# Optimization experiments

Hardware: AMD Instinct MI355X
Metric: run time of the kernel (lower is better)

Reference implementation:

```python
import jax, jax.numpy as jnp
import numpy as np

N = 8192
IN_F = 512
OUT_F = 256
EDGE_P = 0.02  # adjacency density


def setup_inputs() -> dict:
    key = jax.random.key(0)
    k1, k2, k3, k4 = jax.random.split(key, 4)
    x = jax.random.normal(k1, (N, IN_F), dtype=jnp.float32)
    # xavier_uniform with gain=1.414 ~ std gain*sqrt(2/(fan_in+fan_out))
    W = jax.random.normal(k2, (IN_F, OUT_F), dtype=jnp.float32) * (1.414 * np.sqrt(2.0 / (IN_F + OUT_F)))
    a = jax.random.normal(k3, (2 * OUT_F, 1), dtype=jnp.float32) * (1.414 * np.sqrt(2.0 / (2 * OUT_F + 1)))
    adj = (jax.random.uniform(k4, (N, N)) < EDGE_P).astype(jnp.float32)
    return {"x": x, "adj": adj, "W": W, "a": a}


def reference(x, adj, W, a):
    h = x @ W                        # [N, F]
    F = h.shape[1]
    # repeat/cat reduces to an outer sum of two [N] vectors.
    s_src = (h @ a[:F]).squeeze(-1)  # [N], contribution of h_i
    s_dst = (h @ a[F:]).squeeze(-1)  # [N], contribution of h_j
    e = jax.nn.leaky_relu(s_src[:, None] + s_dst[None, :], negative_slope=0.2)  # [N, N]
    # NOTE: original code softmaxes over the FULL row, THEN multiplies by adj.
    attention = jax.nn.softmax(e, axis=1) * adj  # [N, N]
    h_prime = attention @ h                      # [N, F]
    return h_prime, attention
```

## Files before the change

### kernel.cpp

```cpp
#include <hip/hip_runtime.h>
#include <hip/hip_bf16.h>

#define N_NODES 8192
#define IN_F    512
#define OUT_F   256
#define MAXNZ   512

typedef float v4f  __attribute__((ext_vector_type(4)));
typedef __attribute__((ext_vector_type(8)))  short bf16x8;
typedef __attribute__((ext_vector_type(16))) float f32x16;
typedef unsigned short u16;
typedef unsigned int   u32;

__device__ __forceinline__ u16 f2bf(float f) {
  u32 u = __float_as_uint(f);
  u += 0x7fffu + ((u >> 16) & 1u);
  return (u16)(u >> 16);
}
__device__ __forceinline__ float bf2f(u16 h) {
  return __uint_as_float(((u32)h) << 16);
}

__global__ __launch_bounds__(256) void k_cast_x(const float* __restrict__ x,
                                                u16* __restrict__ x_hi,
                                                u16* __restrict__ x_lo) {
  const int idx = blockIdx.x * 256 + threadIdx.x;
  const float4 v = ((const float4*)x)[idx];
  u16 h0 = f2bf(v.x), h1 = f2bf(v.y), h2 = f2bf(v.z), h3 = f2bf(v.w);
  u16 l0 = f2bf(v.x - bf2f(h0)), l1 = f2bf(v.y - bf2f(h1));
  u16 l2 = f2bf(v.z - bf2f(h2)), l3 = f2bf(v.w - bf2f(h3));
  uint2 hp, lp;
  hp.x = (u32)h0 | ((u32)h1 << 16); hp.y = (u32)h2 | ((u32)h3 << 16);
  lp.x = (u32)l0 | ((u32)l1 << 16); lp.y = (u32)l2 | ((u32)l3 << 16);
  ((uint2*)x_hi)[idx] = hp;
  ((uint2*)x_lo)[idx] = lp;
}

__global__ __launch_bounds__(256) void k_cast_wt(const float* __restrict__ W,
                                                 u16* __restrict__ wt_hi,
                                                 u16* __restrict__ wt_lo) {
  const int k = blockIdx.x;
  const int n = threadIdx.x;
  const float v = W[(size_t)k * OUT_F + n];
  const u16 h = f2bf(v);
  wt_hi[(size_t)n * IN_F + k] = h;
  wt_lo[(size_t)n * IN_F + k] = f2bf(v - bf2f(h));
}

#define GBK 64
__global__ __launch_bounds__(256) void k_gemm_mfma(const u16* __restrict__ x_hi,
                                                   const u16* __restrict__ x_lo,
                                                   const u16* __restrict__ wt_hi,
                                                   const u16* __restrict__ wt_lo,
                                                   const float* __restrict__ a,
                                                   u16* __restrict__ h_bf,
                                                   float* __restrict__ s_src,
                                                   float* __restrict__ s_dst) {
  __shared__ u16 As_hi[64 * 68], As_lo[64 * 68], Bs_hi[64 * 68], Bs_lo[64 * 68];
  const int t    = threadIdx.x;
  const int bn   = blockIdx.x & 3;
  const int bm   = blockIdx.x >> 2;
  const int m0   = bm * 64, n0 = bn * 64;
  const int lane = t & 63;
  const int w    = t >> 6;
  const int wm   = w & 1, wn = w >> 1;

  const int sm = t >> 2;
  const int sk = (t & 3) * 16;

  f32x16 acc = {};

  for (int k0 = 0; k0 < IN_F; k0 += GBK) {
#pragma unroll
    for (int i = 0; i < 2; ++i) {
      const int ko = sk + i * 8;
      *(bf16x8*)&As_hi[sm * 68 + ko] = *(const bf16x8*)&x_hi[(size_t)(m0 + sm) * IN_F + k0 + ko];
      *(bf16x8*)&As_lo[sm * 68 + ko] = *(const bf16x8*)&x_lo[(size_t)(m0 + sm) * IN_F + k0 + ko];
      *(bf16x8*)&Bs_hi[sm * 68 + ko] = *(const bf16x8*)&wt_hi[(size_t)(n0 + sm) * IN_F + k0 + ko];
      *(bf16x8*)&Bs_lo[sm * 68 + ko] = *(const bf16x8*)&wt_lo[(size_t)(n0 + sm) * IN_F + k0 + ko];
    }
    __syncthreads();
    const int am  = wm * 32 + (lane & 31);
    const int bn_ = wn * 32 + (lane & 31);
#pragma unroll
    for (int kk = 0; kk < 4; ++kk) {
      const int ko = kk * 16 + (lane >> 5) * 8;
      const bf16x8 ah = *(const bf16x8*)&As_hi[am * 68 + ko];
      const bf16x8 al = *(const bf16x8*)&As_lo[am * 68 + ko];
      const bf16x8 bh = *(const bf16x8*)&Bs_hi[bn_ * 68 + ko];
      const bf16x8 bl = *(const bf16x8*)&Bs_lo[bn_ * 68 + ko];
      acc = __builtin_amdgcn_mfma_f32_32x32x16_bf16(ah, bh, acc, 0, 0, 0);
      acc = __builtin_amdgcn_mfma_f32_32x32x16_bf16(al, bh, acc, 0, 0, 0);
      acc = __builtin_amdgcn_mfma_f32_32x32x16_bf16(ah, bl, acc, 0, 0, 0);
    }
    __syncthreads();
  }
  const int colg = n0 + wn * 32 + (lane & 31);
  const float asv = a[colg];
  const float adv = a[OUT_F + colg];
#pragma unroll
  for (int r = 0; r < 16; ++r) {
    const int row = m0 + wm * 32 + (r & 3) + 8 * (r >> 2) + 4 * (lane >> 5);
    const float v = acc[r];
    h_bf[(size_t)row * OUT_F + colg] = f2bf(v);
    float vs = v * asv, vd = v * adv;
#pragma unroll
    for (int off = 1; off < 32; off <<= 1) {
      vs += __shfl_xor(vs, off);
      vd += __shfl_xor(vd, off);
    }
    if ((lane & 31) == 0) {
      atomicAdd(&s_src[row], vs);
      atomicAdd(&s_dst[row], vd);
    }
  }
}

__device__ __forceinline__ float lrelu_exp(float v) {
  const float e = v > 0.f ? v : 0.2f * v;
  return __expf(e);
}

__global__ __launch_bounds__(256) void k_attn(const float* __restrict__ adj,
                                              const u16* __restrict__ h_bf,
                                              const float* __restrict__ s_src,
                                              const float* __restrict__ s_dst,
                                              float* __restrict__ out_hp,
                                              float* __restrict__ out_att) {
  __shared__ float nza[MAXNZ];
  __shared__ int   nzj[MAXNZ];
  __shared__ float redbuf[4];
  __shared__ int   cnt;

  const int t = threadIdx.x;
  const int i = blockIdx.x;
  const float ssrc = s_src[i];
  if (t == 0) cnt = 0;

  const float4* sd4 = (const float4*)s_dst;
  float4 p[8];
  float lsum = 0.f;
#pragma unroll
  for (int c = 0; c < 8; ++c) {
    const float4 s = sd4[c * 256 + t];
    p[c].x = lrelu_exp(ssrc + s.x);
    p[c].y = lrelu_exp(ssrc + s.y);
    p[c].z = lrelu_exp(ssrc + s.z);
    p[c].w = lrelu_exp(ssrc + s.w);
    lsum += p[c].x + p[c].y + p[c].z + p[c].w;
  }
#pragma unroll
  for (int off = 32; off > 0; off >>= 1) lsum += __shfl_down(lsum, off);
  if ((t & 63) == 0) redbuf[t >> 6] = lsum;
  __syncthreads();
  const float inv = 1.0f / (redbuf[0] + redbuf[1] + redbuf[2] + redbuf[3]);

  const v4f* adj4 = (const v4f*)(adj + (size_t)i * N_NODES);
  v4f*       att4 = (v4f*)(out_att + (size_t)i * N_NODES);
  v4f av[8];
#pragma unroll
  for (int c = 0; c < 8; ++c) av[c] = __builtin_nontemporal_load(adj4 + c * 256 + t);
#pragma unroll
  for (int c = 0; c < 8; ++c) {
    v4f att;
    att.x = av[c].x * (p[c].x * inv);
    att.y = av[c].y * (p[c].y * inv);
    att.z = av[c].z * (p[c].z * inv);
    att.w = av[c].w * (p[c].w * inv);
    __builtin_nontemporal_store(att, att4 + c * 256 + t);
    const int j = (c * 256 + t) * 4;
    if (av[c].x != 0.f) { const int k = atomicAdd(&cnt, 1); if (k < MAXNZ) { nzj[k] = j + 0; nza[k] = att.x; } }
    if (av[c].y != 0.f) { const int k = atomicAdd(&cnt, 1); if (k < MAXNZ) { nzj[k] = j + 1; nza[k] = att.y; } }
    if (av[c].z != 0.f) { const int k = atomicAdd(&cnt, 1); if (k < MAXNZ) { nzj[k] = j + 2; nza[k] = att.z; } }
    if (av[c].w != 0.f) { const int k = atomicAdd(&cnt, 1); if (k < MAXNZ) { nzj[k] = j + 3; nza[k] = att.w; } }
  }
  __syncthreads();

  const int n = cnt < MAXNZ ? cnt : MAXNZ;
  float acc = 0.f;
#pragma unroll 8
  for (int k = 0; k < n; ++k) {
    acc = fmaf(nza[k], bf2f(h_bf[(size_t)nzj[k] * OUT_F + t]), acc);
  }
  out_hp[(size_t)i * OUT_F + t] = acc;
}

extern "C" void kernel_launch(void* const* d_in, const int* in_sizes, int n_in,
                              void* d_out, int out_size, void* d_ws, size_t ws_size,
                              hipStream_t stream) {
  const float* x   = (const float*)d_in[0];
  const float* adj = (const float*)d_in[1];
  const float* W   = (const float*)d_in[2];
  const float* a   = (const float*)d_in[3];

  float* out_hp  = (float*)d_out;
  float* out_att = (float*)d_out + (size_t)N_NODES * OUT_F;

  char* ws = (char*)d_ws;
  float* ssrc_ws = (float*)ws;                       ws += N_NODES * 4;
  float* sdst_ws = (float*)ws;                       ws += N_NODES * 4;
  u16*   x_hi    = (u16*)ws;                         ws += (size_t)N_NODES * IN_F * 2;
  u16*   x_lo    = (u16*)ws;                         ws += (size_t)N_NODES * IN_F * 2;
  u16*   wt_hi   = (u16*)ws;                         ws += (size_t)OUT_F * IN_F * 2;
  u16*   wt_lo   = (u16*)ws;                         ws += (size_t)OUT_F * IN_F * 2;
  u16*   h_bf    = (u16*)ws;                         ws += (size_t)N_NODES * OUT_F * 2;

  hipMemsetAsync(ssrc_ws, 0, 2 * N_NODES * sizeof(float), stream);

  k_cast_x<<<(N_NODES * IN_F / 4) / 256, 256, 0, stream>>>(x, x_hi, x_lo);
  k_cast_wt<<<IN_F, OUT_F, 0, stream>>>(W, wt_hi, wt_lo);
  k_gemm_mfma<<<(N_NODES / 64) * (OUT_F / 64), 256, 0, stream>>>(
      x_hi, x_lo, wt_hi, wt_lo, a, h_bf, ssrc_ws, sdst_ws);
  k_attn<<<N_NODES, 256, 0, stream>>>(adj, h_bf, ssrc_ws, sdst_ws, out_hp, out_att);
}
```

Baseline: 508.1 us.

## Assign one wavefront per attention row and recompute exp instead of caching

The attention kernel now maps each 64-lane wavefront to its own row, so a 256-thread block handles four rows. This removes block-wide __syncthreads and the shared-memory reduction; the softmax sum is reduced with wave shuffles only. Exponentials are computed in a first pass for the sum and computed again in a second pass, which cuts register use but doubles the exp work and the s_dst reads. The sparse aggregation now has each lane accumulate four output features from 8-byte h loads and write them as one float4.

```diff
diff --git a/kernel.cpp b/kernel.cpp
--- a/kernel.cpp
+++ b/kernel.cpp
@@ -127,62 +127,72 @@
                                               const float* __restrict__ s_dst,
                                               float* __restrict__ out_hp,
                                               float* __restrict__ out_att) {
-  __shared__ float nza[MAXNZ];
-  __shared__ int   nzj[MAXNZ];
-  __shared__ float redbuf[4];
-  __shared__ int   cnt;
-
-  const int t = threadIdx.x;
-  const int i = blockIdx.x;
+  __shared__ float nza[4][MAXNZ];
+  __shared__ int   nzj[4][MAXNZ];
+  __shared__ int   cnt[4];
+
+  const int lane = threadIdx.x & 63;
+  const int wid  = threadIdx.x >> 6;
+  const int i    = blockIdx.x * 4 + wid;
   const float ssrc = s_src[i];
-  if (t == 0) cnt = 0;
+  if (lane == 0) cnt[wid] = 0;
 
   const float4* sd4 = (const float4*)s_dst;
-  float4 p[8];
+
   float lsum = 0.f;
-#pragma unroll
-  for (int c = 0; c < 8; ++c) {
-    const float4 s = sd4[c * 256 + t];
-    p[c].x = lrelu_exp(ssrc + s.x);
-    p[c].y = lrelu_exp(ssrc + s.y);
-    p[c].z = lrelu_exp(ssrc + s.z);
-    p[c].w = lrelu_exp(ssrc + s.w);
-    lsum += p[c].x + p[c].y + p[c].z + p[c].w;
+  for (int c0 = 0; c0 < 32; c0 += 4) {
+    float4 s[4];
+#pragma unroll
+    for (int u = 0; u < 4; ++u) s[u] = sd4[(c0 + u) * 64 + lane];
+#pragma unroll
+    for (int u = 0; u < 4; ++u) {
+      lsum += lrelu_exp(ssrc + s[u].x) + lrelu_exp(ssrc + s[u].y)
+            + lrelu_exp(ssrc + s[u].z) + lrelu_exp(ssrc + s[u].w);
+    }
   }
 #pragma unroll
   for (int off = 32; off > 0; off >>= 1) lsum += __shfl_down(lsum, off);
-  if ((t & 63) == 0) redbuf[t >> 6] = lsum;
-  __syncthreads();
-  const float inv = 1.0f / (redbuf[0] + redbuf[1] + redbuf[2] + redbuf[3]);
+  const float inv = 1.0f / __shfl(lsum, 0);
 
   const v4f* adj4 = (const v4f*)(adj + (size_t)i * N_NODES);
   v4f*       att4 = (v4f*)(out_att + (size_t)i * N_NODES);
-  v4f av[8];
-#pragma unroll
-  for (int c = 0; c < 8; ++c) av[c] = __builtin_nontemporal_load(adj4 + c * 256 + t);
-#pragma unroll
-  for (int c = 0; c < 8; ++c) {
-    v4f att;
-    att.x = av[c].x * (p[c].x * inv);
-    att.y = av[c].y * (p[c].y * inv);
-    att.z = av[c].z * (p[c].z * inv);
-    att.w = av[c].w * (p[c].w * inv);
-    __builtin_nontemporal_store(att, att4 + c * 256 + t);
-    const int j = (c * 256 + t) * 4;
-    if (av[c].x != 0.f) { const int k = atomicAdd(&cnt, 1); if (k < MAXNZ) { nzj[k] = j + 0; nza[k] = att.x; } }
-    if (av[c].y != 0.f) { const int k = atomicAdd(&cnt, 1); if (k < MAXNZ) { nzj[k] = j + 1; nza[k] = att.y; } }
-    if (av[c].z != 0.f) { const int k = atomicAdd(&cnt, 1); if (k < MAXNZ) { nzj[k] = j + 2; nza[k] = att.z; } }
-    if (av[c].w != 0.f) { const int k = atomicAdd(&cnt, 1); if (k < MAXNZ) { nzj[k] = j + 3; nza[k] = att.w; } }
-  }
-  __syncthreads();
-
-  const int n = cnt < MAXNZ ? cnt : MAXNZ;
-  float acc = 0.f;
+  for (int c0 = 0; c0 < 32; c0 += 4) {
+    v4f   av[4];
+    float4 s[4];
+#pragma unroll
+    for (int u = 0; u < 4; ++u) av[u] = __builtin_nontemporal_load(adj4 + (c0 + u) * 64 + lane);
+#pragma unroll
+    for (int u = 0; u < 4; ++u) s[u] = sd4[(c0 + u) * 64 + lane];
+#pragma unroll
+    for (int u = 0; u < 4; ++u) {
+      v4f att;
+      att.x = av[u].x * (lrelu_exp(ssrc + s[u].x) * inv);
+      att.y = av[u].y * (lrelu_exp(ssrc + s[u].y) * inv);
+      att.z = av[u].z * (lrelu_exp(ssrc + s[u].z) * inv);
+      att.w = av[u].w * (lrelu_exp(ssrc + s[u].w) * inv);
+      __builtin_nontemporal_store(att, att4 + (c0 + u) * 64 + lane);
+      const int j = ((c0 + u) * 64 + lane) * 4;
+      if (av[u].x != 0.f) { const int k = atomicAdd(&cnt[wid], 1); if (k < MAXNZ) { nzj[wid][k] = j + 0; nza[wid][k] = att.x; } }
+      if (av[u].y != 0.f) { const int k = atomicAdd(&cnt[wid], 1); if (k < MAXNZ) { nzj[wid][k] = j + 1; nza[wid][k] = att.y; } }
+      if (av[u].z != 0.f) { const int k = atomicAdd(&cnt[wid], 1); if (k < MAXNZ) { nzj[wid][k] = j + 2; nza[wid][k] = att.z; } }
+      if (av[u].w != 0.f) { const int k = atomicAdd(&cnt[wid], 1); if (k < MAXNZ) { nzj[wid][k] = j + 3; nza[wid][k] = att.w; } }
+    }
+  }
+
+  const int n = cnt[wid] < MAXNZ ? cnt[wid] : MAXNZ;
+  float a0 = 0.f, a1 = 0.f, a2 = 0.f, a3 = 0.f;
 #pragma unroll 8
   for (int k = 0; k < n; ++k) {
-    acc = fmaf(nza[k], bf2f(h_bf[(size_t)nzj[k] * OUT_F + t]), acc);
-  }
-  out_hp[(size_t)i * OUT_F + t] = acc;
+    const int   j = nzj[wid][k];
+    const float w = nza[wid][k];
+    const uint2 hv = *(const uint2*)&h_bf[(size_t)j * OUT_F + lane * 4];
+    a0 = fmaf(w, bf2f((u16)(hv.x & 0xffffu)), a0);
+    a1 = fmaf(w, bf2f((u16)(hv.x >> 16)),     a1);
+    a2 = fmaf(w, bf2f((u16)(hv.y & 0xffffu)), a2);
+    a3 = fmaf(w, bf2f((u16)(hv.y >> 16)),     a3);
+  }
+  float4 o; o.x = a0; o.y = a1; o.z = a2; o.w = a3;
+  *(float4*)&out_hp[(size_t)i * OUT_F + lane * 4] = o;
 }
 
 extern "C" void kernel_launch(void* const* d_in, const int* in_sizes, int n_in,
@@ -211,5 +221,5 @@
   k_cast_wt<<<IN_F, OUT_F, 0, stream>>>(W, wt_hi, wt_lo);
   k_gemm_mfma<<<(N_NODES / 64) * (OUT_F / 64), 256, 0, stream>>>(
       x_hi, x_lo, wt_hi, wt_lo, a, h_bf, ssrc_ws, sdst_ws);
-  k_attn<<<N_NODES, 256, 0, stream>>>(adj, h_bf, ssrc_ws, sdst_ws, out_hp, out_att);
-}
+  k_attn<<<N_NODES / 4, 256, 0, stream>>>(adj, h_bf, ssrc_ws, sdst_ws, out_hp, out_att);
+}
```

Result: no change. 513.9 us (+1.1%).
